# Performance work log

Measured on AMD Instinct MI355X. Metric: run time of the kernel, lower is better.

Reference implementation:

```python
import jax, jax.numpy as jnp
import numpy as np

LMAX = 4
S2_DIM = (LMAX + 1) ** 2                                  # 25: s2 irreps, mul 1 per l
SO3_DIM = sum((2 * l + 1) ** 2 for l in range(LMAX + 1))  # 165: so3 irreps, mul 2l+1 per l
B = 2048
F_S2, F_SO3 = 1, 16
N_S2_KERNEL = 48      # s2_healpix_grid(rec_level=1)
N_SO3_KERNEL = 192    # so3_near_identity_grid()
N_ACT_GRID = 4000     # SO3Activation resolution=10, aspect_ratio=2 -> 20x10x20, flattened
N_EVAL = 4608         # so3_healpix_grid(rec_level=2): 192 pixels x 24 gamma


def setup_inputs() -> dict:
    ks = jax.random.split(jax.random.key(0), 7)
    return {
        "x": jax.random.normal(ks[0], (B, F_S2, S2_DIM), jnp.float32),
        "w_s2": jax.random.normal(ks[1], (F_S2, F_SO3, N_S2_KERNEL), jnp.float32),
        "Y": jax.random.normal(ks[2], (N_S2_KERNEL, S2_DIM), jnp.float32),
        "w_so3": jax.random.normal(ks[3], (F_SO3, 1, N_SO3_KERNEL), jnp.float32),
        "D_kernel": jax.random.normal(ks[4], (N_SO3_KERNEL, SO3_DIM), jnp.float32),
        "D_act": jax.random.normal(ks[5], (N_ACT_GRID, SO3_DIM), jnp.float32),
        "eval_wigners": jax.random.normal(ks[6], (SO3_DIM, N_EVAL), jnp.float32) / np.sqrt(SO3_DIM),
    }


def _s2_to_so3_linear(x, psi):
    # e3nn o3.Linear(s2_irreps -> so3_irreps, f_in, f_out, external weights)
    # x:   [B, f_in, 25]  (mul 1 per degree l)
    # psi: [f_in, f_out, 25] ; column l^2+j is the weight to output-multiplicity j of degree l
    f_in, f_out = psi.shape[0], psi.shape[1]
    out, s = [], 0
    for l in range(LMAX + 1):
        d = 2 * l + 1
        x_l = x[..., s:s + d]                       # [B, f_in, d]
        p_l = psi[..., s:s + d]                     # [f_in, f_out, d] (j = out-mul idx)
        o = jnp.einsum('bxm,xyj->byjm', x_l, p_l) / np.sqrt(f_in)
        out.append(o.reshape(x.shape[0], f_out, d * d))
        s += d
    return jnp.concatenate(out, axis=-1)            # [B, f_out, 165]


def _so3_to_so3_linear(x, psi):
    # e3nn o3.Linear(so3_irreps -> so3_irreps, f_in, f_out, external weights)
    # x:   [B, f_in, 165] ; psi: [f_in, f_out, 165]
    f_in, f_out = psi.shape[0], psi.shape[1]
    out, s = [], 0
    for l in range(LMAX + 1):
        d = 2 * l + 1
        x_l = x[..., s:s + d * d].reshape(x.shape[0], f_in, d, d)   # [B,f_in,u,m]
        p_l = psi[..., s:s + d * d].reshape(f_in, f_out, d, d)      # [f_in,f_out,u,v]
        o = jnp.einsum('bxum,xyuv->byvm', x_l, p_l) / np.sqrt(f_in * d)
        out.append(o.reshape(x.shape[0], f_out, d * d))
        s += d * d
    return jnp.concatenate(out, axis=-1)            # [B, f_out, 165]


def _forward(x, w_s2, Y, w_so3, D_kernel, D_act, eval_wigners):
    # --- S2Convolution: kernel = SH-transform of grid weights, then irrep-wise linear
    psi1 = jnp.einsum('ni,xyn->xyi', Y, w_s2) / np.sqrt(N_S2_KERNEL)     # [1,16,25]
    h = _s2_to_so3_linear(x, psi1)                                        # [B,16,165]
    # --- SO3Activation: Fourier -> SO(3) grid -> relu -> Fourier
    g = jnp.einsum('bfi,gi->bfg', h, D_act) / np.sqrt(SO3_DIM)            # [B,16,4000]
    g = jax.nn.relu(g)
    h = jnp.einsum('bfg,gi->bfi', g, D_act) * (np.sqrt(SO3_DIM) / N_ACT_GRID)
    # --- SO3Convolution
    psi2 = jnp.einsum('ni,xyn->xyi', D_kernel, w_so3) / np.sqrt(N_SO3_KERNEL)  # [16,1,165]
    harmonics = _so3_to_so3_linear(h, psi2)                               # [B,1,165]
    # --- compute_probabilities: matmul with eval Wigner-D basis + softmax over grid
    probs = jax.nn.softmax(jnp.einsum('bfi,ie->be', harmonics, eval_wigners), axis=1)  # [B,4608]
    # --- top-k masking: zero out everything below the 5th-highest prob of sample 0
    fifth = jax.lax.top_k(probs, 5)[0][0, 4]
    probs = jnp.where(probs < fifth, 0.0, probs)
    return harmonics, probs


def reference(x, w_s2, Y, w_so3, D_kernel, D_act, eval_wigners):
    return _forward(x, w_s2, Y, w_so3, D_kernel, D_act, eval_wigners)
```

## Files before the change

kernel.cpp:

```cpp
#include <hip/hip_runtime.h>

typedef short bf16x8 __attribute__((ext_vector_type(8)));
typedef float f32x16 __attribute__((ext_vector_type(16)));
typedef int   i32x4  __attribute__((ext_vector_type(4)));

#define INV_SQRT165 0.07784989441615349f
#define FINAL_SCALE 0.0032113081446662823f
#define ZERO16 ((f32x16){0.f,0.f,0.f,0.f,0.f,0.f,0.f,0.f,0.f,0.f,0.f,0.f,0.f,0.f,0.f,0.f})

__device__ __forceinline__ unsigned short f2bf(float f) {
  unsigned int u = __builtin_bit_cast(unsigned int, f);
  unsigned int r = (u + 0x7FFFu + ((u >> 16) & 1u)) >> 16;
  return (unsigned short)r;
}
__device__ __forceinline__ float bf2f(unsigned short h) {
  unsigned int u = ((unsigned int)h) << 16;
  return __builtin_bit_cast(float, u);
}

__device__ __forceinline__ void gl_lds16(const void* g, void* l) {
  __builtin_amdgcn_global_load_lds(
      (const __attribute__((address_space(1))) unsigned int*)(unsigned long long)g,
      (__attribute__((address_space(3))) unsigned int*)(unsigned int)(unsigned long long)l,
      16, 0, 0);
}

__device__ __forceinline__ void decode_i(int i, int& lv, int& rel) {
  if (i < 1)       { lv = 0; rel = i; }
  else if (i < 10) { lv = 1; rel = i - 1; }
  else if (i < 35) { lv = 2; rel = i - 10; }
  else if (i < 84) { lv = 3; rel = i - 35; }
  else             { lv = 4; rel = i - 84; }
}
__device__ __forceinline__ int divq(int rel, int lv) {
  const int mag[5] = {32768, 10923, 6554, 4682, 3641};
  return (rel * mag[lv]) >> 15;
}

__device__ __forceinline__ int gperm(int p) {
  int a = p & 3, hlp = (p >> 2) & 1, c = p >> 3;
  return ((c >> 1) << 4) + hlp * 8 + ((c & 1) << 2) + a;
}

__global__ __launch_bounds__(256) void prep_k(const float* __restrict__ Da,
                                              const float* __restrict__ ew,
                                              const float* __restrict__ Y,
                                              const float* __restrict__ w_s2,
                                              const float* __restrict__ Dk,
                                              const float* __restrict__ w_so3,
                                              unsigned short* __restrict__ e1pre,
                                              unsigned short* __restrict__ d2pre,
                                              unsigned short* __restrict__ ewpre,
                                              float* __restrict__ psi2) {
  __shared__ __align__(16) unsigned short lds[13824];
  const int tid = threadIdx.x;
  const int l = tid & 63, hl = l >> 5, ln = l & 31;
  if (blockIdx.x < 512) {
    const int ci = blockIdx.x >> 2, yg = blockIdx.x & 3;
    const int g0 = ci * 32;
    float* psi1L = (float*)(lds + 6464);
    for (int e = tid; e < 6400; e += 256) lds[e] = 0;
    for (int e = tid; e < 400; e += 256) {
      int yv = e / 25, iv = e % 25;
      float s = 0.f;
      for (int n = 0; n < 48; n++) s += Y[n * 25 + iv] * w_s2[yv * 48 + n];
      psi1L[e] = s * 0.14433756729740643f;
    }
    __syncthreads();
    int rows = 4000 - g0; if (rows > 32) rows = 32; if (rows < 0) rows = 0;
    int ne = rows * 165;
    for (int e = tid; e < ne; e += 256) {
      int gl_ = e / 165, k = e - gl_ * 165;
      lds[gl_ * 200 + k] = f2bf(Da[g0 * 165 + e]);
    }
    __syncthreads();
    if (yg == 0) {
#pragma unroll
      for (int it = 0; it < 3; it++) {
        int tt = it * 4 + (tid >> 6);
        int nf = tt >> 1, gk = tt & 1;
        unsigned short v[8];
#pragma unroll
        for (int j = 0; j < 8; j++)
          v[j] = lds[(gk * 16 + hl * 8 + j) * 200 + nf * 32 + ln];
        *(i32x4*)(d2pre + ci * 6144 + tt * 512 + l * 8) = *(i32x4*)v;
      }
    }
    for (int yi = 0; yi < 4; yi++) {
      int yy = yg * 4 + yi;
#pragma unroll
      for (int it = 0; it < 4; it++) {
        int idx = it * 256 + tid;
        int kf = idx >> 9, r2 = idx & 511;
        int ll = r2 >> 3, j = r2 & 7;
        int lnn = ll & 31, hll = ll >> 5;
        int k = kf * 16 + hll * 8 + j;
        unsigned short ov = 0;
        if (k < 25) {
          int lv = (k < 1) ? 0 : (k < 4) ? 1 : (k < 9) ? 2 : (k < 16) ? 3 : 4;
          int d = 2 * lv + 1;
          int m = k - lv * lv;
          int off165 = lv * (4 * lv * lv - 1) / 3;
          int gp = gperm(lnn);
          float s = 0.f;
          const float* pr = psi1L + yy * 25 + lv * lv;
          const unsigned short* dr = lds + gp * 200 + off165 + m;
          for (int j2 = 0; j2 < d; j2++) s += pr[j2] * bf2f(dr[j2 * d]);
          ov = f2bf(s * INV_SQRT165);
        }
        e1pre[((yy * 128 + ci) * 2 + kf) * 512 + ll * 8 + j] = ov;
      }
    }
  } else if (blockIdx.x < 584) {
    const int bx2 = blockIdx.x - 512;
    const int n0 = bx2 * 64;
    for (int e = tid; e < 13824; e += 256) lds[e] = 0;
    __syncthreads();
    for (int e = tid; e < 10560; e += 256) {
      int k = e >> 6, n = e & 63;
      lds[k * 72 + n] = f2bf(ew[k * 4608 + n0 + n]);
    }
    __syncthreads();
#pragma unroll
    for (int it = 0; it < 6; it++) {
      int tb = it * 4 + (tid >> 6);
      int nt2 = tb / 12, kf = tb - nt2 * 12;
      unsigned short v[8];
#pragma unroll
      for (int j = 0; j < 8; j++)
        v[j] = lds[(kf * 16 + hl * 8 + j) * 72 + nt2 * 32 + ln];
      *(i32x4*)(ewpre + (bx2 * 2 + nt2) * 6144 + kf * 512 + l * 8) = *(i32x4*)v;
    }
  } else {
    int t = (blockIdx.x - 584) * 256 + tid;
    if (t < 2640) {
      int ch = t / 165, i = t % 165;
      float s = 0.f;
      for (int n = 0; n < 192; n++) s += Dk[n * 165 + i] * w_so3[ch * 192 + n];
      psi2[t] = s * (0.07216878364870323f * FINAL_SCALE);
    }
  }
}

__global__ __launch_bounds__(256, 2) void fused_mlp_k(
    const float* __restrict__ x,
    const unsigned short* __restrict__ e1pre,
    const unsigned short* __restrict__ d2pre,
    unsigned short* __restrict__ part)
{
  __shared__ __align__(16) unsigned char smem[49152];
  const int tid = threadIdx.x;
  const int w = tid >> 6, l = tid & 63;
  const int hl = l >> 5, ln = l & 31;
  const int h = blockIdx.x >> 8;
  const int y = (blockIdx.x >> 4) & 15;
  const int btg = blockIdx.x & 15;
  const int bt = btg * 4 + w;
  const int c0 = h * 63;
  const int cnt = h ? 62 : 63;

  bf16x8 xf[2];
  {
    const float* xr = x + (bt * 32 + ln) * 25;
#pragma unroll
    for (int kf = 0; kf < 2; kf++) {
      unsigned short v[8];
#pragma unroll
      for (int j = 0; j < 8; j++) {
        int k = kf * 16 + hl * 8 + j;
        v[j] = (k < 25) ? f2bf(xr[k]) : (unsigned short)0;
      }
      xf[kf] = *(bf16x8*)v;
    }
  }

  f32x16 o[6];
#pragma unroll
  for (int i = 0; i < 6; i++) o[i] = ZERO16;

  const unsigned short* ebase = e1pre + (y * 128) * 1024;

#define STAGE(lc, buf) do {                                               \
    unsigned char* nb_ = smem + (buf) * 16384;                            \
    const int c_ = c0 + (lc);                                             \
    _Pragma("unroll")                                                     \
    for (int i_ = 0; i_ < 4; i_++) {                                      \
      int tb_ = w * 4 + i_;                                               \
      int st_ = (tb_ < 14) ? tb_ : (tb_ - 14);                            \
      const unsigned short* src_ = (st_ < 2)                              \
          ? ebase + c_ * 1024 + st_ * 512 + l * 8                         \
          : d2pre + c_ * 6144 + (st_ - 2) * 512 + l * 8;                  \
      gl_lds16(src_, nb_ + tb_ * 1024);                                   \
    }                                                                     \
  } while (0)

#define COMPUTE(cbp) do {                                                  \
    const unsigned char* cb_ = (cbp);                                      \
    bf16x8 eC0 = *(const bf16x8*)(cb_ + l * 16);                           \
    bf16x8 eC1 = *(const bf16x8*)(cb_ + 1024 + l * 16);                    \
    f32x16 s = ZERO16;                                                     \
    s = __builtin_amdgcn_mfma_f32_32x32x16_bf16(eC0, xf[0], s, 0, 0, 0);   \
    s = __builtin_amdgcn_mfma_f32_32x32x16_bf16(eC1, xf[1], s, 0, 0, 0);   \
    unsigned int dw[8];                                                    \
    _Pragma("unroll")                                                      \
    for (int p_ = 0; p_ < 8; p_++) {                                       \
      float lo = fmaxf(s[2 * p_], 0.f), hi = fmaxf(s[2 * p_ + 1], 0.f);    \
      asm("v_cvt_pk_bf16_f32 %0, %1, %2" : "=v"(dw[p_]) : "v"(lo), "v"(hi)); \
    }                                                                      \
    bf16x8 a20 = __builtin_bit_cast(bf16x8,                                \
        (i32x4){(int)dw[0], (int)dw[1], (int)dw[2], (int)dw[3]});          \
    bf16x8 a21 = __builtin_bit_cast(bf16x8,                                \
        (i32x4){(int)dw[4], (int)dw[5], (int)dw[6], (int)dw[7]});          \
    _Pragma("unroll")                                                      \
    for (int gk = 0; gk < 2; gk++) {                                       \
      bf16x8 a2 = gk ? a21 : a20;                                          \
      _Pragma("unroll")                                                    \
      for (int nf = 0; nf < 6; nf++) {                                     \
        bf16x8 b2 = *(const bf16x8*)(cb_ + 2048 + (nf * 2 + gk) * 1024 + l * 16); \
        o[nf] = __builtin_amdgcn_mfma_f32_32x32x16_bf16(a2, b2, o[nf], 0, 0, 0);  \
      }                                                                    \
    }                                                                      \
  } while (0)

  STAGE(0, 0);
  STAGE(1, 1);

  int bufc = 0;
  for (int ci = 0; ci < cnt - 1; ci++) {
    asm volatile("s_waitcnt vmcnt(4)" ::: "memory");
    asm volatile("s_waitcnt lgkmcnt(0)" ::: "memory");
    __builtin_amdgcn_s_barrier();
    if (ci + 2 < cnt) {
      int bn = bufc + 2; if (bn >= 3) bn -= 3;
      STAGE(ci + 2, bn);
    }
    COMPUTE(smem + bufc * 16384);
    bufc = (bufc == 2) ? 0 : bufc + 1;
  }
  asm volatile("s_waitcnt vmcnt(0)" ::: "memory");
  asm volatile("s_waitcnt lgkmcnt(0)" ::: "memory");
  __builtin_amdgcn_s_barrier();
  COMPUTE(smem + bufc * 16384);

#undef STAGE
#undef COMPUTE

  unsigned short* pp = part + (size_t)((h * 16 + y) * 2048 + bt * 32) * 192;
#pragma unroll
  for (int nf = 0; nf < 6; nf++) {
    int n = nf * 32 + ln;
    if (n < 176) {
#pragma unroll
      for (int r = 0; r < 16; r++) {
        int row = (r & 3) + 8 * (r >> 2) + 4 * hl;
        pp[row * 192 + n] = f2bf(o[nf][r]);
      }
    }
  }
}

__global__ __launch_bounds__(256) void so3_k(const unsigned short* __restrict__ part,
                                             const float* __restrict__ psi2,
                                             float* __restrict__ harm_out,
                                             unsigned short* __restrict__ harmbpre) {
  __shared__ float lds[4 * 16 * 180];
  __shared__ float p2s[2640];
  const int tid = threadIdx.x;
  const int b0 = blockIdx.x * 4;
  for (int e = tid; e < 2640; e += 256) p2s[e] = psi2[e];
  {
    const int ybl = tid >> 2;
    const int yy = ybl & 15, bloc = ybl >> 4;
    const int s = tid & 3;
    const unsigned int* r0 = (const unsigned int*)(part + ((size_t)(0 * 16 + yy) * 2048 + b0 + bloc) * 192);
    const unsigned int* r1 = (const unsigned int*)(part + ((size_t)(1 * 16 + yy) * 2048 + b0 + bloc) * 192);
    float* dst = lds + (bloc * 16 + yy) * 180;
#pragma unroll
    for (int t = 0; t < 22; t++) {
      int d = s * 22 + t;
      if (d < 88) {
        unsigned int u0 = r0[d], u1 = r1[d];
        int n0 = d * 2;
        dst[n0]     = bf2f((unsigned short)(u0 & 0xFFFF)) + bf2f((unsigned short)(u1 & 0xFFFF));
        dst[n0 + 1] = bf2f((unsigned short)(u0 >> 16)) + bf2f((unsigned short)(u1 >> 16));
      }
    }
  }
  __syncthreads();
  for (int jj = tid; jj < 768; jj += 256) {
    int e = (jj * 683) >> 17;
    int i = jj - e * 192;
    int bb = b0 + e;
    unsigned short* hb = harmbpre + (((bb >> 5) * 12 + (i >> 4)) << 9)
                       + ((i >> 3) & 1) * 256 + (bb & 31) * 8 + (i & 7);
    if (i < 165) {
      const float* row0 = lds + e * (16 * 180);
      int lv, rel; decode_i(i, lv, rel);
      int d = 2 * lv + 1;
      int off = i - rel;
      int v = divq(rel, lv), m = rel - v * d;
      float s = 0.f;
      for (int ch = 0; ch < 16; ch++) {
        const float* rw = row0 + ch * 180 + off;
        const float* p2 = p2s + ch * 165 + off;
        for (int u = 0; u < d; u++) s += rw[u * d + m] * p2[u * d + v];
      }
      s *= 0.25f * rsqrtf((float)d);
      harm_out[bb * 165 + i] = s;
      *hb = f2bf(s);
    } else {
      *hb = 0;
    }
  }
}

__global__ __launch_bounds__(64) void eval_k(
    const unsigned short* __restrict__ harmbpre,
    const unsigned short* __restrict__ ewpre,
    float* __restrict__ logits,
    float* __restrict__ logit0)
{
  const int l = threadIdx.x;
  const int hl = l >> 5, ln = l & 31;
  const int mt = blockIdx.y;
  const int n0 = blockIdx.x * 192;

  bf16x8 a[12];
  const short* ap = (const short*)harmbpre + mt * 6144 + l * 8;
#pragma unroll
  for (int kf = 0; kf < 12; kf++) a[kf] = *(const bf16x8*)(ap + kf * 512);

  f32x16 acc[6];
#pragma unroll
  for (int nf = 0; nf < 6; nf++) acc[nf] = ZERO16;

  const short* bp = (const short*)ewpre + (blockIdx.x * 6) * 6144 + l * 8;
#pragma unroll
  for (int kf = 0; kf < 12; kf++) {
#pragma unroll
    for (int nf = 0; nf < 6; nf++) {
      bf16x8 b = *(const bf16x8*)(bp + nf * 6144 + kf * 512);
      acc[nf] = __builtin_amdgcn_mfma_f32_32x32x16_bf16(a[kf], b, acc[nf], 0, 0, 0);
    }
  }
#pragma unroll
  for (int nf = 0; nf < 6; nf++) {
    const int col = n0 + nf * 32 + ln;
#pragma unroll
    for (int r = 0; r < 16; r++) {
      int row = (r & 3) + 8 * (r >> 2) + 4 * hl;
      logits[(mt * 32 + row) * 4608 + col] = acc[nf][r];
    }
  }
  if (mt == 0 && hl == 0) {
#pragma unroll
    for (int nf = 0; nf < 6; nf++) logit0[n0 + nf * 32 + ln] = acc[nf][0];
  }
}

__global__ __launch_bounds__(256) void fifth_k(const float* __restrict__ logit0,
                                               float* __restrict__ fifth) {
  __shared__ float buf[4608];
  __shared__ float sm[4], ss[4];
  __shared__ float wv[4]; __shared__ int wi[4];
  __shared__ float gbest;
  const int tid = threadIdx.x;
  const int l = tid & 63, w = tid >> 6;
  float v[18];
  float mx = -3.4e38f;
#pragma unroll
  for (int i = 0; i < 18; i++) {
    v[i] = logit0[i * 256 + tid];
    buf[i * 256 + tid] = v[i];
    mx = fmaxf(mx, v[i]);
  }
#pragma unroll
  for (int off = 32; off >= 1; off >>= 1) mx = fmaxf(mx, __shfl_xor(mx, off));
  if (l == 0) sm[w] = mx;
  __syncthreads();
  mx = fmaxf(fmaxf(sm[0], sm[1]), fmaxf(sm[2], sm[3]));
  float s = 0.f;
#pragma unroll
  for (int i = 0; i < 18; i++) s += __expf(v[i] - mx);
#pragma unroll
  for (int off = 32; off >= 1; off >>= 1) s += __shfl_xor(s, off);
  if (l == 0) ss[w] = s;
  __syncthreads();
  s = ss[0] + ss[1] + ss[2] + ss[3];
  float inv = 1.f / s;

  float ff = 0.f;
  for (int it = 0; it < 5; it++) {
    float bm = -3.4e38f; int bi = 0;
    for (int i = tid; i < 4608; i += 256) {
      float xx = buf[i];
      if (xx > bm) { bm = xx; bi = i; }
    }
    for (int off = 32; off >= 1; off >>= 1) {
      float ov = __shfl_xor(bm, off); int oi = __shfl_xor(bi, off);
      if (ov > bm) { bm = ov; bi = oi; }
    }
    if (l == 0) { wv[w] = bm; wi[w] = bi; }
    __syncthreads();
    if (tid == 0) {
      float B = wv[0]; int I = wi[0];
      for (int k = 1; k < 4; k++) if (wv[k] > B) { B = wv[k]; I = wi[k]; }
      gbest = B;
      buf[I] = -3.4e38f;
    }
    __syncthreads();
    ff = gbest;
    __syncthreads();
  }
  if (tid == 0) *fifth = __expf(ff - mx) * inv;
}

__global__ __launch_bounds__(256) void smthresh_k(float* __restrict__ probs,
                                                  const float* __restrict__ fifth) {
  float* p = probs + (size_t)blockIdx.x * 4608;
  const int tid = threadIdx.x;
  const int l = tid & 63, w = tid >> 6;
  __shared__ float sm[4], ss[4];
  float v[18];
  float mx = -3.4e38f;
#pragma unroll
  for (int i = 0; i < 18; i++) { v[i] = p[i * 256 + tid]; mx = fmaxf(mx, v[i]); }
#pragma unroll
  for (int off = 32; off >= 1; off >>= 1) mx = fmaxf(mx, __shfl_xor(mx, off));
  if (l == 0) sm[w] = mx;
  __syncthreads();
  mx = fmaxf(fmaxf(sm[0], sm[1]), fmaxf(sm[2], sm[3]));
  float s = 0.f;
#pragma unroll
  for (int i = 0; i < 18; i++) { v[i] = __expf(v[i] - mx); s += v[i]; }
#pragma unroll
  for (int off = 32; off >= 1; off >>= 1) s += __shfl_xor(s, off);
  if (l == 0) ss[w] = s;
  __syncthreads();
  s = ss[0] + ss[1] + ss[2] + ss[3];
  float inv = 1.f / s;
  float t = *fifth;
#pragma unroll
  for (int i = 0; i < 18; i++) {
    float pv = v[i] * inv;
    p[i * 256 + tid] = (pv < t) ? 0.f : pv;
  }
}

extern "C" void kernel_launch(void* const* d_in, const int* in_sizes, int n_in,
                              void* d_out, int out_size, void* d_ws, size_t ws_size,
                              hipStream_t stream) {
  const float* x     = (const float*)d_in[0];
  const float* w_s2  = (const float*)d_in[1];
  const float* Y     = (const float*)d_in[2];
  const float* w_so3 = (const float*)d_in[3];
  const float* Dk    = (const float*)d_in[4];
  const float* Da    = (const float*)d_in[5];
  const float* ew    = (const float*)d_in[6];

  float* out = (float*)d_out;
  float* harm_out = out;
  float* probs    = out + 337920;
  unsigned short* part = (unsigned short*)probs;

  char* ws = (char*)d_ws;
  float* psi2  = (float*)(ws + 0);
  float* fifth = (float*)(ws + 10560);
  unsigned short* e1pre    = (unsigned short*)(ws + 12288);
  unsigned short* d2pre    = (unsigned short*)(ws + 4206592);
  unsigned short* ewpre    = (unsigned short*)(ws + 5779456);
  unsigned short* harmbpre = (unsigned short*)(ws + 7548928);
  float* logit0 = (float*)(ws + 8335360);

  prep_k<<<595, 256, 0, stream>>>(Da, ew, Y, w_s2, Dk, w_so3, e1pre, d2pre, ewpre, psi2);
  fused_mlp_k<<<512, 256, 0, stream>>>(x, e1pre, d2pre, part);
  so3_k<<<512, 256, 0, stream>>>(part, psi2, harm_out, harmbpre);
  eval_k<<<dim3(24, 64), 64, 0, stream>>>(harmbpre, ewpre, probs, logit0);
  fifth_k<<<1, 256, 0, stream>>>(logit0, fifth);
  smthresh_k<<<2048, 256, 0, stream>>>(probs, fifth);
}
```

Baseline: 214.1 us.

## Split fused MLP output columns across wave pairs with per-wave LDS double buffers

Each block now has 2 batch tiles by 2 output halves instead of 4 batch tiles with all 6 output fragments, so the grid doubles to 1024 blocks. Each wave stages its own first-layer and half-second-layer tiles into a private double buffer, which removes the block-wide barriers and lgkmcnt waits. The cost is duplicated loads of the shared first-layer tiles and 64KB of LDS per block, which reduces how many blocks can be resident per CU. Per-wave accumulators shrink from 6 to 3 fragments, lowering register pressure.

```diff
diff --git a/kernel.cpp b/kernel.cpp
--- a/kernel.cpp
+++ b/kernel.cpp
@@ -148,16 +148,19 @@
     const unsigned short* __restrict__ d2pre,
     unsigned short* __restrict__ part)
 {
-  __shared__ __align__(16) unsigned char smem[49152];
+  __shared__ __align__(16) unsigned char smem[65536];
   const int tid = threadIdx.x;
   const int w = tid >> 6, l = tid & 63;
   const int hl = l >> 5, ln = l & 31;
-  const int h = blockIdx.x >> 8;
-  const int y = (blockIdx.x >> 4) & 15;
-  const int btg = blockIdx.x & 15;
-  const int bt = btg * 4 + w;
+  const int h = blockIdx.x >> 9;
+  const int y = (blockIdx.x >> 5) & 15;
+  const int btg = blockIdx.x & 31;
+  const int btp = w >> 1, nh = w & 1;
+  const int bt = btg * 2 + btp;
   const int c0 = h * 63;
   const int cnt = h ? 62 : 63;
+
+  unsigned char* wbuf = smem + w * 16384;
 
   bf16x8 xf[2];
   {
@@ -174,28 +177,25 @@
     }
   }
 
-  f32x16 o[6];
-#pragma unroll
-  for (int i = 0; i < 6; i++) o[i] = ZERO16;
+  f32x16 o[3];
+#pragma unroll
+  for (int i = 0; i < 3; i++) o[i] = ZERO16;
 
   const unsigned short* ebase = e1pre + (y * 128) * 1024;
 
-#define STAGE(lc, buf) do {                                               \
-    unsigned char* nb_ = smem + (buf) * 16384;                            \
-    const int c_ = c0 + (lc);                                             \
-    _Pragma("unroll")                                                     \
-    for (int i_ = 0; i_ < 4; i_++) {                                      \
-      int tb_ = w * 4 + i_;                                               \
-      int st_ = (tb_ < 14) ? tb_ : (tb_ - 14);                            \
-      const unsigned short* src_ = (st_ < 2)                              \
-          ? ebase + c_ * 1024 + st_ * 512 + l * 8                         \
-          : d2pre + c_ * 6144 + (st_ - 2) * 512 + l * 8;                  \
-      gl_lds16(src_, nb_ + tb_ * 1024);                                   \
-    }                                                                     \
+#define STAGE(lc, bi) do {                                                 \
+    unsigned char* nb_ = wbuf + (bi) * 8192;                               \
+    const int c_ = c0 + (lc);                                              \
+    gl_lds16(ebase + c_ * 1024 + l * 8, nb_);                              \
+    gl_lds16(ebase + c_ * 1024 + 512 + l * 8, nb_ + 1024);                 \
+    _Pragma("unroll")                                                      \
+    for (int j_ = 0; j_ < 6; j_++)                                         \
+      gl_lds16(d2pre + c_ * 6144 + (nh * 6 + j_) * 512 + l * 8,            \
+               nb_ + 2048 + j_ * 1024);                                    \
   } while (0)
 
-#define COMPUTE(cbp) do {                                                  \
-    const unsigned char* cb_ = (cbp);                                      \
+#define COMPUTE(bi) do {                                                   \
+    const unsigned char* cb_ = wbuf + (bi) * 8192;                         \
     bf16x8 eC0 = *(const bf16x8*)(cb_ + l * 16);                           \
     bf16x8 eC1 = *(const bf16x8*)(cb_ + 1024 + l * 16);                    \
     f32x16 s = ZERO16;                                                     \
@@ -215,7 +215,7 @@
     for (int gk = 0; gk < 2; gk++) {                                       \
       bf16x8 a2 = gk ? a21 : a20;                                          \
       _Pragma("unroll")                                                    \
-      for (int nf = 0; nf < 6; nf++) {                                     \
+      for (int nf = 0; nf < 3; nf++) {                                     \
         bf16x8 b2 = *(const bf16x8*)(cb_ + 2048 + (nf * 2 + gk) * 1024 + l * 16); \
         o[nf] = __builtin_amdgcn_mfma_f32_32x32x16_bf16(a2, b2, o[nf], 0, 0, 0);  \
       }                                                                    \
@@ -223,32 +223,21 @@
   } while (0)
 
   STAGE(0, 0);
-  STAGE(1, 1);
-
-  int bufc = 0;
   for (int ci = 0; ci < cnt - 1; ci++) {
-    asm volatile("s_waitcnt vmcnt(4)" ::: "memory");
-    asm volatile("s_waitcnt lgkmcnt(0)" ::: "memory");
-    __builtin_amdgcn_s_barrier();
-    if (ci + 2 < cnt) {
-      int bn = bufc + 2; if (bn >= 3) bn -= 3;
-      STAGE(ci + 2, bn);
-    }
-    COMPUTE(smem + bufc * 16384);
-    bufc = (bufc == 2) ? 0 : bufc + 1;
+    STAGE(ci + 1, (ci + 1) & 1);
+    asm volatile("s_waitcnt vmcnt(8)" ::: "memory");
+    COMPUTE(ci & 1);
   }
   asm volatile("s_waitcnt vmcnt(0)" ::: "memory");
-  asm volatile("s_waitcnt lgkmcnt(0)" ::: "memory");
-  __builtin_amdgcn_s_barrier();
-  COMPUTE(smem + bufc * 16384);
+  COMPUTE((cnt - 1) & 1);
 
 #undef STAGE
 #undef COMPUTE
 
   unsigned short* pp = part + (size_t)((h * 16 + y) * 2048 + bt * 32) * 192;
 #pragma unroll
-  for (int nf = 0; nf < 6; nf++) {
-    int n = nf * 32 + ln;
+  for (int nf = 0; nf < 3; nf++) {
+    int n = nh * 96 + nf * 32 + ln;
     if (n < 176) {
 #pragma unroll
       for (int r = 0; r < 16; r++) {
@@ -473,7 +462,7 @@
   float* logit0 = (float*)(ws + 8335360);
 
   prep_k<<<595, 256, 0, stream>>>(Da, ew, Y, w_s2, Dk, w_so3, e1pre, d2pre, ewpre, psi2);
-  fused_mlp_k<<<512, 256, 0, stream>>>(x, e1pre, d2pre, part);
+  fused_mlp_k<<<1024, 256, 0, stream>>>(x, e1pre, d2pre, part);
   so3_k<<<512, 256, 0, stream>>>(part, psi2, harm_out, harmbpre);
   eval_k<<<dim3(24, 64), 64, 0, stream>>>(harmbpre, ewpre, probs, logit0);
   fifth_k<<<1, 256, 0, stream>>>(logit0, fifth);
```

New measurement: 241.1 us. 1.13x slower.

## Replace logits round-trip with two-pass online softmax recomputing GEMM

Applied to the files above, without the earlier changes.

The first GEMM pass now writes only per-row, per-column-block max and sum-of-exp partial statistics instead of the full 2048x4608 logits matrix. A single-block finalize kernel merges the partials into row max and inverse sum, and also computes the top-5 threshold from row 0. A second GEMM pass recomputes the logits and writes normalized, thresholded probabilities directly. This removes the write and re-read of the full logits array in exchange for running the bf16 MFMA GEMM twice and adding a serial per-row merge loop inside a single-block kernel.

```diff
diff --git a/kernel.cpp b/kernel.cpp
--- a/kernel.cpp
+++ b/kernel.cpp
@@ -314,16 +314,16 @@
   }
 }
 
-__global__ __launch_bounds__(64) void eval_k(
+__global__ __launch_bounds__(64) void evalA_k(
     const unsigned short* __restrict__ harmbpre,
     const unsigned short* __restrict__ ewpre,
-    float* __restrict__ logits,
+    float* __restrict__ stats,
     float* __restrict__ logit0)
 {
   const int l = threadIdx.x;
   const int hl = l >> 5, ln = l & 31;
   const int mt = blockIdx.y;
-  const int n0 = blockIdx.x * 192;
+  const int cb = blockIdx.x;
 
   bf16x8 a[12];
   const short* ap = (const short*)harmbpre + mt * 6144 + l * 8;
@@ -334,7 +334,7 @@
 #pragma unroll
   for (int nf = 0; nf < 6; nf++) acc[nf] = ZERO16;
 
-  const short* bp = (const short*)ewpre + (blockIdx.x * 6) * 6144 + l * 8;
+  const short* bp = (const short*)ewpre + (cb * 6) * 6144 + l * 8;
 #pragma unroll
   for (int kf = 0; kf < 12; kf++) {
 #pragma unroll
@@ -343,29 +343,50 @@
       acc[nf] = __builtin_amdgcn_mfma_f32_32x32x16_bf16(a[kf], b, acc[nf], 0, 0, 0);
     }
   }
-#pragma unroll
-  for (int nf = 0; nf < 6; nf++) {
-    const int col = n0 + nf * 32 + ln;
-#pragma unroll
-    for (int r = 0; r < 16; r++) {
-      int row = (r & 3) + 8 * (r >> 2) + 4 * hl;
-      logits[(mt * 32 + row) * 4608 + col] = acc[nf][r];
-    }
-  }
   if (mt == 0 && hl == 0) {
 #pragma unroll
-    for (int nf = 0; nf < 6; nf++) logit0[n0 + nf * 32 + ln] = acc[nf][0];
-  }
-}
-
-__global__ __launch_bounds__(256) void fifth_k(const float* __restrict__ logit0,
-                                               float* __restrict__ fifth) {
+    for (int nf = 0; nf < 6; nf++) logit0[cb * 192 + nf * 32 + ln] = acc[nf][0];
+  }
+#pragma unroll
+  for (int r = 0; r < 16; r++) {
+    int row = (r & 3) + 8 * (r >> 2) + 4 * hl;
+    float m = acc[0][r];
+#pragma unroll
+    for (int nf = 1; nf < 6; nf++) m = fmaxf(m, acc[nf][r]);
+#pragma unroll
+    for (int off = 16; off >= 1; off >>= 1) m = fmaxf(m, __shfl_xor(m, off));
+    float s = 0.f;
+#pragma unroll
+    for (int nf = 0; nf < 6; nf++) s += __expf(acc[nf][r] - m);
+#pragma unroll
+    for (int off = 16; off >= 1; off >>= 1) s += __shfl_xor(s, off);
+    if (ln == 0) {
+      float2 v2; v2.x = m; v2.y = s;
+      *(float2*)&stats[((mt * 32 + row) * 24 + cb) * 2] = v2;
+    }
+  }
+}
+
+__global__ __launch_bounds__(256) void finalize_k(const float* __restrict__ logit0,
+                                                  const float* __restrict__ stats,
+                                                  float* __restrict__ rowstats,
+                                                  float* __restrict__ fifth) {
   __shared__ float buf[4608];
   __shared__ float sm[4], ss[4];
   __shared__ float wv[4]; __shared__ int wi[4];
   __shared__ float gbest;
   const int tid = threadIdx.x;
   const int l = tid & 63, w = tid >> 6;
+  for (int row = tid; row < 2048; row += 256) {
+    const float2* st = (const float2*)(stats + row * 48);
+    float M = -3.4e38f;
+#pragma unroll
+    for (int j = 0; j < 24; j++) M = fmaxf(M, st[j].x);
+    float S = 0.f;
+#pragma unroll
+    for (int j = 0; j < 24; j++) { float2 v = st[j]; S += v.y * __expf(v.x - M); }
+    rowstats[row * 2] = M; rowstats[row * 2 + 1] = 1.f / S;
+  }
   float v[18];
   float mx = -3.4e38f;
 #pragma unroll
@@ -388,6 +409,7 @@
   __syncthreads();
   s = ss[0] + ss[1] + ss[2] + ss[3];
   float inv = 1.f / s;
+  if (tid == 0) { rowstats[0] = mx; rowstats[1] = inv; }
 
   float ff = 0.f;
   for (int it = 0; it < 5; it++) {
@@ -415,35 +437,48 @@
   if (tid == 0) *fifth = __expf(ff - mx) * inv;
 }
 
-__global__ __launch_bounds__(256) void smthresh_k(float* __restrict__ probs,
-                                                  const float* __restrict__ fifth) {
-  float* p = probs + (size_t)blockIdx.x * 4608;
-  const int tid = threadIdx.x;
-  const int l = tid & 63, w = tid >> 6;
-  __shared__ float sm[4], ss[4];
-  float v[18];
-  float mx = -3.4e38f;
-#pragma unroll
-  for (int i = 0; i < 18; i++) { v[i] = p[i * 256 + tid]; mx = fmaxf(mx, v[i]); }
-#pragma unroll
-  for (int off = 32; off >= 1; off >>= 1) mx = fmaxf(mx, __shfl_xor(mx, off));
-  if (l == 0) sm[w] = mx;
-  __syncthreads();
-  mx = fmaxf(fmaxf(sm[0], sm[1]), fmaxf(sm[2], sm[3]));
-  float s = 0.f;
-#pragma unroll
-  for (int i = 0; i < 18; i++) { v[i] = __expf(v[i] - mx); s += v[i]; }
-#pragma unroll
-  for (int off = 32; off >= 1; off >>= 1) s += __shfl_xor(s, off);
-  if (l == 0) ss[w] = s;
-  __syncthreads();
-  s = ss[0] + ss[1] + ss[2] + ss[3];
-  float inv = 1.f / s;
-  float t = *fifth;
-#pragma unroll
-  for (int i = 0; i < 18; i++) {
-    float pv = v[i] * inv;
-    p[i * 256 + tid] = (pv < t) ? 0.f : pv;
+__global__ __launch_bounds__(64) void probsC_k(
+    const unsigned short* __restrict__ harmbpre,
+    const unsigned short* __restrict__ ewpre,
+    const float* __restrict__ rowstats,
+    const float* __restrict__ fifth,
+    float* __restrict__ probs)
+{
+  const int l = threadIdx.x;
+  const int hl = l >> 5, ln = l & 31;
+  const int mt = blockIdx.y;
+  const int n0 = blockIdx.x * 192;
+
+  bf16x8 a[12];
+  const short* ap = (const short*)harmbpre + mt * 6144 + l * 8;
+#pragma unroll
+  for (int kf = 0; kf < 12; kf++) a[kf] = *(const bf16x8*)(ap + kf * 512);
+
+  f32x16 acc[6];
+#pragma unroll
+  for (int nf = 0; nf < 6; nf++) acc[nf] = ZERO16;
+
+  const short* bp = (const short*)ewpre + (blockIdx.x * 6) * 6144 + l * 8;
+#pragma unroll
+  for (int kf = 0; kf < 12; kf++) {
+#pragma unroll
+    for (int nf = 0; nf < 6; nf++) {
+      bf16x8 b = *(const bf16x8*)(bp + nf * 6144 + kf * 512);
+      acc[nf] = __builtin_amdgcn_mfma_f32_32x32x16_bf16(a[kf], b, acc[nf], 0, 0, 0);
+    }
+  }
+  const float t = *fifth;
+#pragma unroll
+  for (int r = 0; r < 16; r++) {
+    int row = (r & 3) + 8 * (r >> 2) + 4 * hl;
+    int grow = mt * 32 + row;
+    float2 ms = *(const float2*)&rowstats[grow * 2];
+    float* pr = probs + (size_t)grow * 4608 + n0;
+#pragma unroll
+    for (int nf = 0; nf < 6; nf++) {
+      float pv = __expf(acc[nf][r] - ms.x) * ms.y;
+      pr[nf * 32 + ln] = (pv < t) ? 0.f : pv;
+    }
   }
 }
 
@@ -462,6 +497,7 @@
   float* harm_out = out;
   float* probs    = out + 337920;
   unsigned short* part = (unsigned short*)probs;
+  float* stats    = probs;
 
   char* ws = (char*)d_ws;
   float* psi2  = (float*)(ws + 0);
@@ -470,12 +506,13 @@
   unsigned short* d2pre    = (unsigned short*)(ws + 4206592);
   unsigned short* ewpre    = (unsigned short*)(ws + 5779456);
   unsigned short* harmbpre = (unsigned short*)(ws + 7548928);
-  float* logit0 = (float*)(ws + 8335360);
+  float* logit0   = (float*)(ws + 8335360);
+  float* rowstats = (float*)(ws + 8353792);
 
   prep_k<<<595, 256, 0, stream>>>(Da, ew, Y, w_s2, Dk, w_so3, e1pre, d2pre, ewpre, psi2);
   fused_mlp_k<<<512, 256, 0, stream>>>(x, e1pre, d2pre, part);
   so3_k<<<512, 256, 0, stream>>>(part, psi2, harm_out, harmbpre);
-  eval_k<<<dim3(24, 64), 64, 0, stream>>>(harmbpre, ewpre, probs, logit0);
-  fifth_k<<<1, 256, 0, stream>>>(logit0, fifth);
-  smthresh_k<<<2048, 256, 0, stream>>>(probs, fifth);
-}
+  evalA_k<<<dim3(24, 64), 64, 0, stream>>>(harmbpre, ewpre, stats, logit0);
+  finalize_k<<<1, 256, 0, stream>>>(logit0, stats, rowstats, fifth);
+  probsC_k<<<dim3(24, 64), 64, 0, stream>>>(harmbpre, ewpre, rowstats, fifth, probs);
+}
```

Measured after the change: 226.3 us. 1.06x slower.
